# Performance work log

Hardware: AMD Instinct MI355X
Metric: run time of the kernel (lower is better)

The kernel has to match this reference:

```python
import jax, jax.numpy as jnp
import numpy as np
import math

B, C, H, W = 32, 3, 512, 512
K = 16
OUT_H, OUT_W = 512, 512

def _ctrl_pts(k):
    gs = int(math.sqrt(k))
    lin = jnp.linspace(-1.0, 1.0, gs)
    gy, gx = jnp.meshgrid(lin, lin, indexing='ij')
    return jnp.stack([gx, gy], axis=-1).reshape(-1, 2)

def setup_inputs() -> dict:
    key = jax.random.key(0)
    k1, k2, k3, k4 = jax.random.split(key, 4)
    x = jax.random.normal(k1, (B, C, H, W), jnp.float32)
    conv_w = jax.random.normal(k2, (8, C, 7, 7), jnp.float32) * 0.05
    conv_b = jax.random.normal(k3, (8,), jnp.float32) * 0.05
    fc_w = jax.random.normal(k4, (2 * K, 8), jnp.float32) * 0.01
    fc_b = jnp.asarray(_ctrl_pts(K).reshape(-1))  # module inits bias to ctrl grid
    return {"x": x, "conv_w": conv_w, "conv_b": conv_b, "fc_w": fc_w, "fc_b": fc_b}

def _U(sq):
    # U(r) = r^2 * log(r^2 + 1e-6), expressed with squared distance sq = r^2
    return sq * jnp.log(sq + 1e-6)

def _tps_grid(src, tgt, out_h, out_w):
    # src: [K,2] shared across batch (fixed ctrl grid), tgt: [B,K,2]
    Bb, Kk, _ = tgt.shape
    lin_y = jnp.linspace(-1.0, 1.0, out_h)
    lin_x = jnp.linspace(-1.0, 1.0, out_w)
    gy, gx = jnp.meshgrid(lin_y, lin_x, indexing='ij')
    grid = jnp.stack([gx, gy], axis=-1).reshape(-1, 2)  # [N,2]
    N = out_h * out_w
    # RBF kernel between output grid and source ctrl pts: [N,K]
    d2 = jnp.sum((grid[:, None, :] - src[None, :, :]) ** 2, axis=-1)
    U = _U(d2)
    # TPS system matrix L [K+3,K+3]; src is batch-shared so build it once
    src_d2 = jnp.sum((src[:, None, :] - src[None, :, :]) ** 2, axis=-1)
    P = jnp.concatenate([jnp.ones((Kk, 1)), src], axis=1)  # [K,3]
    L = jnp.zeros((Kk + 3, Kk + 3))
    L = L.at[:Kk, :Kk].set(_U(src_d2))
    L = L.at[:Kk, Kk:].set(P)
    L = L.at[Kk:, :Kk].set(P.T)
    Y = jnp.concatenate([tgt, jnp.zeros((Bb, 3, 2))], axis=1)  # [B,K+3,2]
    Wmat = jnp.linalg.solve(L[None], Y)  # [B,K+3,2]
    Pg = jnp.concatenate([jnp.ones((N, 1)), grid], axis=1)  # [N,3]
    mapped = (jnp.einsum('nk,bkc->bnc', U, Wmat[:, :Kk])
              + jnp.einsum('np,bpc->bnc', Pg, Wmat[:, Kk:]))
    return mapped.reshape(Bb, out_h, out_w, 2)

def _grid_sample(x, grid):
    # bilinear, zero padding, align_corners=False (torch defaults)
    Bb, Cc, Hh, Ww = x.shape
    ix = ((grid[..., 0] + 1.0) * Ww - 1.0) * 0.5
    iy = ((grid[..., 1] + 1.0) * Hh - 1.0) * 0.5
    x0 = jnp.floor(ix)
    y0 = jnp.floor(iy)
    wx1 = ix - x0
    wy1 = iy - y0
    x0i = x0.astype(jnp.int32)
    y0i = y0.astype(jnp.int32)

    def gather(img, yy, xx):
        valid = ((yy >= 0) & (yy < Hh) & (xx >= 0) & (xx < Ww)).astype(img.dtype)
        yc = jnp.clip(yy, 0, Hh - 1)
        xc = jnp.clip(xx, 0, Ww - 1)
        return img[:, yc, xc] * valid[None]

    def per(img, x0i, y0i, wx1, wy1):
        wx0 = 1.0 - wx1
        wy0 = 1.0 - wy1
        v00 = gather(img, y0i, x0i)
        v01 = gather(img, y0i, x0i + 1)
        v10 = gather(img, y0i + 1, x0i)
        v11 = gather(img, y0i + 1, x0i + 1)
        return (v00 * (wy0 * wx0)[None] + v01 * (wy0 * wx1)[None]
                + v10 * (wy1 * wx0)[None] + v11 * (wy1 * wx1)[None])

    return jax.vmap(per)(x, x0i, y0i, wx1, wy1)

def reference(x, conv_w, conv_b, fc_w, fc_b):
    # localization: conv7x7 -> relu -> global avg pool -> fc
    feat = jax.lax.conv_general_dilated(
        x, conv_w, window_strides=(1, 1), padding='VALID',
        dimension_numbers=('NCHW', 'OIHW', 'NCHW'))
    feat = jax.nn.relu(feat + conv_b[None, :, None, None])
    pooled = feat.mean(axis=(2, 3))  # [B,8] (AdaptiveAvgPool2d(1))
    pred = (pooled @ fc_w.T + fc_b).reshape(-1, K, 2)  # [B,K,2]
    src = _ctrl_pts(K)
    grid = _tps_grid(src, pred, OUT_H, OUT_W)  # [B,OUT_H,OUT_W,2]
    return _grid_sample(x, grid)
```

## Files before the change

kernel.cpp:

```cpp
#include <hip/hip_runtime.h>
#include <hip/hip_bf16.h>
#include <hip/hip_fp16.h>
#include <math.h>

#define BATCH 32
#define CH_IN 3
#define CH_OUT 8
#define IMG 512
#define KSZ 7
#define CONV_OUT 506
#define KPTS 16
#define TILES_PER_B 128

#define SROWS 23
#define ROW_U4 24
#define ROW_BYTES 384
#define DATA_U4 19
#define SMEM_DW (CH_IN * SROWS * ROW_U4 * 4)
#define NCHUNK (CH_IN * SROWS * ROW_U4)

#define BPB 8

typedef _Float16 half8_t __attribute__((ext_vector_type(8)));
typedef float f32x4_t __attribute__((ext_vector_type(4)));

__device__ __forceinline__ unsigned short f2h_bits(float f) {
    _Float16 h = (_Float16)f;
    unsigned short u;
    __builtin_memcpy(&u, &h, 2);
    return u;
}
__device__ __forceinline__ float h2f_bits(unsigned short u) {
    _Float16 h;
    __builtin_memcpy(&h, &u, 2);
    return (float)h;
}
__device__ __forceinline__ unsigned int pk2(float a, float b) {
    return (unsigned int)f2h_bits(a) | ((unsigned int)f2h_bits(b) << 16);
}

__global__ void wprep_kernel(const float* __restrict__ w, uint4* __restrict__ afrag) {
    int idx = blockIdx.x * 256 + threadIdx.x;
    if (idx >= 6 * 64) return;
    int s = idx >> 6, l = idx & 63;
    int m = l & 15;
    int dlt = m >> 3, o = m & 7;
    int oct = s * 4 + (l >> 4);
    int c = oct >> 3, ky = oct & 7;
    unsigned short h[8];
    #pragma unroll
    for (int j = 0; j < 8; ++j) {
        int kx = j - dlt;
        float v = 0.f;
        if (ky < KSZ && kx >= 0 && kx < KSZ)
            v = w[((o * CH_IN + c) * KSZ + ky) * KSZ + kx];
        h[j] = f2h_bits(v);
    }
    uint4 out;
    __builtin_memcpy(&out, h, 16);
    afrag[idx] = out;
}

template <bool FUSED>
__global__ __launch_bounds__(256)
void conv_pool_kernel(const float* __restrict__ x, unsigned short* __restrict__ xh,
                      const uint4* __restrict__ afrag, const float* __restrict__ conv_b,
                      float* __restrict__ partial) {
    __shared__ unsigned int smem[SMEM_DW];
    __shared__ float red[4][8];

    int blk = blockIdx.x;
    int b = blk >> 7;
    int stripe = (blk >> 2) & 31;
    int chunk = blk & 3;
    int ybase = stripe * 16;
    int x0 = chunk * 128;
    int tid = threadIdx.x;

    {
        const float* xb = x + (size_t)b * CH_IN * IMG * IMG;
        unsigned short* xhb = xh + (size_t)b * CH_IN * IMG * IMG;
        for (int idx4 = tid; idx4 < NCHUNK; idx4 += 256) {
            int c = idx4 / (SROWS * ROW_U4);
            int rem = idx4 - c * (SROWS * ROW_U4);
            int r = rem / ROW_U4;
            int u4 = rem - r * ROW_U4;
            int grow = ybase + r;
            int gcol = x0 + (u4 << 3);
            uint4 v = make_uint4(0u, 0u, 0u, 0u);
            if (u4 < DATA_U4 && grow < IMG && gcol < IMG) {
                const float* rp = xb + ((size_t)c * IMG + grow) * IMG + gcol;
                float4 f0 = *(const float4*)rp;
                float4 f1 = *(const float4*)(rp + 4);
                v.x = pk2(f0.x, f0.y);
                v.y = pk2(f0.z, f0.w);
                v.z = pk2(f1.x, f1.y);
                v.w = pk2(f1.z, f1.w);
            }
            int row = c * SROWS + r;
            *(uint4*)((char*)smem + row * ROW_BYTES + ((u4 ^ (row & 7)) << 4)) = v;
            if (FUSED && r < 16 && u4 < 16)
                *(uint4*)(xhb + ((size_t)c * IMG + grow) * IMG + gcol) = v;
        }
    }
    __syncthreads();

    int l = tid & 63, w = tid >> 6;
    int n = l & 15, g = l >> 4;

    uint4 at[6];
    #pragma unroll
    for (int s = 0; s < 6; ++s) at[s] = afrag[s * 64 + l];

    int rowB[6], rxb[6];
    #pragma unroll
    for (int s = 0; s < 6; ++s) {
        int oct = s * 4 + g;
        int c = oct >> 3, ky = oct & 7;
        int row = c * SROWS + n + ky;
        rowB[s] = row * ROW_BYTES;
        rxb[s] = (row & 7) << 4;
    }

    float bias_[4];
    {
        int ob = (g & 1) * 4;
        #pragma unroll
        for (int r2 = 0; r2 < 4; ++r2) bias_[r2] = conv_b[ob + r2];
    }
    bool rowok = (ybase + n) < CONV_OUT;
    int dlt = g >> 1;
    float sums[4] = {0.f, 0.f, 0.f, 0.f};
    const char* sb = (const char*)smem;

    #pragma unroll
    for (int u = 0; u < 4; ++u) {
        f32x4_t acc[4];
        #pragma unroll
        for (int d = 0; d < 4; ++d) acc[d] = (f32x4_t){0.f, 0.f, 0.f, 0.f};

        int k0 = (4 * w + u) << 4;
        #pragma unroll
        for (int s = 0; s < 6; ++s) {
            uint4 lo = *(const uint4*)(sb + rowB[s] + (k0 ^ rxb[s]));
            uint4 hi = *(const uint4*)(sb + rowB[s] + ((k0 + 16) ^ rxb[s]));
            unsigned int eu[8] = {lo.x, lo.y, lo.z, lo.w, hi.x, hi.y, hi.z, hi.w};
            half8_t a;
            __builtin_memcpy(&a, &at[s], 16);
            #pragma unroll
            for (int d = 0; d < 4; ++d) {
                uint4 bu = make_uint4(eu[d], eu[d + 1], eu[d + 2], eu[d + 3]);
                half8_t bf;
                __builtin_memcpy(&bf, &bu, 16);
                acc[d] = __builtin_amdgcn_mfma_f32_16x16x32_f16(a, bf, acc[d], 0, 0, 0);
            }
        }

        #pragma unroll
        for (int d = 0; d < 4; ++d) {
            int col = x0 + 32 * w + 8 * u + 2 * d + dlt;
            bool colok = col < CONV_OUT;
            #pragma unroll
            for (int r2 = 0; r2 < 4; ++r2) {
                float v = acc[d][r2] + bias_[r2];
                v = v > 0.f ? v : 0.f;
                sums[r2] += (rowok && colok) ? v : 0.f;
            }
        }
    }

    #pragma unroll
    for (int r2 = 0; r2 < 4; ++r2) {
        sums[r2] += __shfl_xor(sums[r2], 1, 64);
        sums[r2] += __shfl_xor(sums[r2], 2, 64);
        sums[r2] += __shfl_xor(sums[r2], 4, 64);
        sums[r2] += __shfl_xor(sums[r2], 8, 64);
        sums[r2] += __shfl_xor(sums[r2], 32, 64);
    }
    if (l == 0) {
        #pragma unroll
        for (int r2 = 0; r2 < 4; ++r2) red[w][r2] = sums[r2];
    }
    if (l == 16) {
        #pragma unroll
        for (int r2 = 0; r2 < 4; ++r2) red[w][4 + r2] = sums[r2];
    }
    __syncthreads();
    if (tid < CH_OUT) {
        float s = red[0][tid] + red[1][tid] + red[2][tid] + red[3][tid];
        partial[tid * (BATCH * TILES_PER_B) + b * TILES_PER_B + stripe * 4 + chunk] = s;
    }
}

__device__ __forceinline__ double ctrl_lin(int i) { return -1.0 + (2.0 / 3.0) * i; }

__global__ void solve_kernel(const float* __restrict__ partial,
                             const float* __restrict__ fc_w,
                             const float* __restrict__ fc_b,
                             float* __restrict__ Wf) {
    __shared__ double L[19][19];
    __shared__ double Ys[19][64];
    __shared__ double piv_fac[19];
    __shared__ int piv_idx;
    __shared__ float pooledS[BATCH][CH_OUT];

    int t = threadIdx.x;

    for (int p = t; p < BATCH * CH_OUT; p += 64) {
        int b = p >> 3, o = p & 7;
        const float4* pp = (const float4*)(partial + o * (BATCH * TILES_PER_B) + b * TILES_PER_B);
        double a0 = 0.0, a1 = 0.0, a2 = 0.0, a3 = 0.0;
        #pragma unroll
        for (int gq = 0; gq < TILES_PER_B / 4; ++gq) {
            float4 v = pp[gq];
            a0 += (double)v.x; a1 += (double)v.y;
            a2 += (double)v.z; a3 += (double)v.w;
        }
        pooledS[b][o] = (float)(((a0 + a1) + (a2 + a3)) / ((double)CONV_OUT * (double)CONV_OUT));
    }
    __syncthreads();

    {
        int b = t >> 1, c = t & 1;
        for (int k = 0; k < KPTS; ++k) {
            int j = k * 2 + c;
            double s = (double)fc_b[j];
            for (int o = 0; o < CH_OUT; ++o)
                s += (double)pooledS[b][o] * (double)fc_w[j * CH_OUT + o];
            Ys[k][t] = s;
        }
        for (int k = KPTS; k < 19; ++k) Ys[k][t] = 0.0;
    }

    for (int p = t; p < 19 * 19; p += 64) {
        int r = p / 19, cc = p % 19;
        double v;
        if (r < KPTS && cc < KPTS) {
            double dx = ctrl_lin(r & 3) - ctrl_lin(cc & 3);
            double dy = ctrl_lin(r >> 2) - ctrl_lin(cc >> 2);
            double d2 = dx * dx + dy * dy;
            v = d2 * log(d2 + 1e-6);
        } else if (r < KPTS) {
            v = (cc == KPTS) ? 1.0 : (cc == KPTS + 1 ? ctrl_lin(r & 3) : ctrl_lin(r >> 2));
        } else if (cc < KPTS) {
            v = (r == KPTS) ? 1.0 : (r == KPTS + 1 ? ctrl_lin(cc & 3) : ctrl_lin(cc >> 2));
        } else v = 0.0;
        L[r][cc] = v;
    }
    __syncthreads();

    for (int k = 0; k < 19; ++k) {
        if (t == 0) {
            int pi = k; double mx = fabs(L[k][k]);
            for (int i = k + 1; i < 19; ++i) {
                double a = fabs(L[i][k]);
                if (a > mx) { mx = a; pi = i; }
            }
            piv_idx = pi;
        }
        __syncthreads();
        int pi = piv_idx;
        if (pi != k) {
            if (t < 19) { double tmp = L[k][t]; L[k][t] = L[pi][t]; L[pi][t] = tmp; }
            { double tmp = Ys[k][t]; Ys[k][t] = Ys[pi][t]; Ys[pi][t] = tmp; }
        }
        __syncthreads();
        if (t > k && t < 19) piv_fac[t] = L[t][k] / L[k][k];
        __syncthreads();
        if (t > k && t < 19) {
            double lkj = L[k][t];
            for (int i = k + 1; i < 19; ++i) L[i][t] -= piv_fac[i] * lkj;
        }
        {
            double ykt = Ys[k][t];
            for (int i = k + 1; i < 19; ++i) Ys[i][t] -= piv_fac[i] * ykt;
        }
        __syncthreads();
    }

    for (int k = 18; k >= 0; --k) {
        double s = Ys[k][t];
        for (int j = k + 1; j < 19; ++j) s -= L[k][j] * Ys[j][t];
        Ys[k][t] = s / L[k][k];
    }

    {
        int b = t >> 1, c = t & 1;
        for (int k = 0; k < 19; ++k)
            Wf[(b * 19 + k) * 2 + c] = (float)Ys[k][t];
    }
}

template <bool H16>
__global__ __launch_bounds__(256)
void tps_sample_kernel(const float* __restrict__ x, const unsigned short* __restrict__ xh,
                       const float* __restrict__ Wf, float* __restrict__ out) {
    int blk = blockIdx.x;
    int bgrp = blk >> 10;
    int pix = ((blk & 1023) << 8) | threadIdx.x;
    int i = pix >> 9, j = pix & 511;

    float gx = -1.f + (2.f / 511.f) * (float)j;
    float gy = -1.f + (2.f / 511.f) * (float)i;

    float U[KPTS];
    #pragma unroll
    for (int k = 0; k < KPTS; ++k) {
        float sx = -1.f + (2.f / 3.f) * (float)(k & 3);
        float sy = -1.f + (2.f / 3.f) * (float)(k >> 2);
        float dx = gx - sx, dy = gy - sy;
        float d2 = dx * dx + dy * dy;
        U[k] = d2 * (0.69314718055994531f * __log2f(d2 + 1e-6f));
    }

    for (int b = bgrp * BPB; b < bgrp * BPB + BPB; ++b) {
        const float* Wb = Wf + b * 38;

        float mx = Wb[32] + gx * Wb[34] + gy * Wb[36];
        float my = Wb[33] + gx * Wb[35] + gy * Wb[37];
        #pragma unroll
        for (int k = 0; k < KPTS; ++k) {
            mx += U[k] * Wb[2 * k];
            my += U[k] * Wb[2 * k + 1];
        }

        float ix = (mx + 1.f) * 256.f - 0.5f;
        float iy = (my + 1.f) * 256.f - 0.5f;
        float x0f = floorf(ix), y0f = floorf(iy);
        int x0 = (int)x0f, y0 = (int)y0f;
        int x1 = x0 + 1, y1 = y0 + 1;
        float wx1 = ix - x0f, wy1 = iy - y0f;
        float wx0 = 1.f - wx1, wy0 = 1.f - wy1;

        bool vx0 = (x0 >= 0) & (x0 < IMG), vx1 = (x1 >= 0) & (x1 < IMG);
        bool vy0 = (y0 >= 0) & (y0 < IMG), vy1 = (y1 >= 0) & (y1 < IMG);
        int xc0 = min(max(x0, 0), IMG - 1), xc1 = min(max(x1, 0), IMG - 1);
        int yc0 = min(max(y0, 0), IMG - 1), yc1 = min(max(y1, 0), IMG - 1);

        float w00 = (vy0 && vx0) ? wy0 * wx0 : 0.f;
        float w01 = (vy0 && vx1) ? wy0 * wx1 : 0.f;
        float w10 = (vy1 && vx0) ? wy1 * wx0 : 0.f;
        float w11 = (vy1 && vx1) ? wy1 * wx1 : 0.f;

        int o00 = yc0 * IMG + xc0, o01 = yc0 * IMG + xc1;
        int o10 = yc1 * IMG + xc0, o11 = yc1 * IMG + xc1;

        #pragma unroll
        for (int c = 0; c < CH_IN; ++c) {
            float v;
            if (H16) {
                const unsigned short* xp = xh + ((size_t)b * CH_IN + c) * IMG * IMG;
                v = h2f_bits(xp[o00]) * w00 + h2f_bits(xp[o01]) * w01
                  + h2f_bits(xp[o10]) * w10 + h2f_bits(xp[o11]) * w11;
            } else {
                const float* xp = x + ((size_t)b * CH_IN + c) * IMG * IMG;
                v = xp[o00] * w00 + xp[o01] * w01 + xp[o10] * w10 + xp[o11] * w11;
            }
            out[(((size_t)b * CH_IN + c) << 18) + (i << 9) + j] = v;
        }
    }
}

extern "C" void kernel_launch(void* const* d_in, const int* in_sizes, int n_in,
                              void* d_out, int out_size, void* d_ws, size_t ws_size,
                              hipStream_t stream) {
    const float* x      = (const float*)d_in[0];
    const float* conv_w = (const float*)d_in[1];
    const float* conv_b = (const float*)d_in[2];
    const float* fc_w   = (const float*)d_in[3];
    const float* fc_b   = (const float*)d_in[4];
    float* out = (float*)d_out;

    char* ws = (char*)d_ws;
    uint4* afrag   = (uint4*)ws;
    float* partial = (float*)(ws + 8192);
    float* Wf      = (float*)(ws + 139264);
    unsigned short* xh = (unsigned short*)(ws + 147456);
    const size_t need = 147456 + (size_t)BATCH * CH_IN * IMG * IMG * 2;
    bool fused = ws_size >= need;

    wprep_kernel<<<dim3(2), dim3(256), 0, stream>>>(conv_w, afrag);
    if (fused) {
        conv_pool_kernel<true><<<dim3(BATCH * TILES_PER_B), dim3(256), 0, stream>>>(
            x, xh, afrag, conv_b, partial);
    } else {
        conv_pool_kernel<false><<<dim3(BATCH * TILES_PER_B), dim3(256), 0, stream>>>(
            x, xh, afrag, conv_b, partial);
    }
    solve_kernel<<<dim3(1), dim3(64), 0, stream>>>(partial, fc_w, fc_b, Wf);
    if (fused) {
        tps_sample_kernel<true><<<dim3(4 * 1024), dim3(256), 0, stream>>>(x, xh, Wf, out);
    } else {
        tps_sample_kernel<false><<<dim3(4 * 1024), dim3(256), 0, stream>>>(x, xh, Wf, out);
    }
}
```

Measured before the change: 157.3 us.

## Widen conv tiles to 256 columns and replace XOR swizzle with padded rows

Each conv/pool block now covers a 16x256 stripe instead of 16x128, which halves the block count and cuts the halo columns reloaded per tile. The XOR-swizzled LDS layout is replaced by rows padded to 528 bytes, which avoids bank conflicts with simpler addressing, and each wave runs two column chunks per block. The partial-sum indexing and the per-batch tile count are updated to match. The cost is more LDS per block and fewer blocks, so there is less parallelism to hide load latency.

```diff
diff --git a/kernel.cpp b/kernel.cpp
--- a/kernel.cpp
+++ b/kernel.cpp
@@ -10,13 +10,13 @@
 #define KSZ 7
 #define CONV_OUT 506
 #define KPTS 16
-#define TILES_PER_B 128
+#define TILES_PER_B 64
 
 #define SROWS 23
-#define ROW_U4 24
-#define ROW_BYTES 384
-#define DATA_U4 19
-#define SMEM_DW (CH_IN * SROWS * ROW_U4 * 4)
+#define ROW_PX 264
+#define ROW_U4 33
+#define ROW_BYTES 528
+#define SMEM_DW (CH_IN * SROWS * (ROW_BYTES / 4))
 #define NCHUNK (CH_IN * SROWS * ROW_U4)
 
 #define BPB 8
@@ -70,11 +70,12 @@
     __shared__ float red[4][8];
 
     int blk = blockIdx.x;
-    int b = blk >> 7;
-    int stripe = (blk >> 2) & 31;
-    int chunk = blk & 3;
+    int b = blk >> 6;
+    int rem0 = blk & 63;
+    int stripe = rem0 >> 1;
+    int half = rem0 & 1;
     int ybase = stripe * 16;
-    int x0 = chunk * 128;
+    int x0 = half * 256;
     int tid = threadIdx.x;
 
     {
@@ -88,7 +89,7 @@
             int grow = ybase + r;
             int gcol = x0 + (u4 << 3);
             uint4 v = make_uint4(0u, 0u, 0u, 0u);
-            if (u4 < DATA_U4 && grow < IMG && gcol < IMG) {
+            if (grow < IMG && gcol < IMG) {
                 const float* rp = xb + ((size_t)c * IMG + grow) * IMG + gcol;
                 float4 f0 = *(const float4*)rp;
                 float4 f1 = *(const float4*)(rp + 4);
@@ -97,9 +98,8 @@
                 v.z = pk2(f1.x, f1.y);
                 v.w = pk2(f1.z, f1.w);
             }
-            int row = c * SROWS + r;
-            *(uint4*)((char*)smem + row * ROW_BYTES + ((u4 ^ (row & 7)) << 4)) = v;
-            if (FUSED && r < 16 && u4 < 16)
+            *(uint4*)((char*)smem + (c * SROWS + r) * ROW_BYTES + (u4 << 4)) = v;
+            if (FUSED && r < 16 && u4 < 32)
                 *(uint4*)(xhb + ((size_t)c * IMG + grow) * IMG + gcol) = v;
         }
     }
@@ -112,14 +112,12 @@
     #pragma unroll
     for (int s = 0; s < 6; ++s) at[s] = afrag[s * 64 + l];
 
-    int rowB[6], rxb[6];
+    int rowb[6];
     #pragma unroll
     for (int s = 0; s < 6; ++s) {
         int oct = s * 4 + g;
         int c = oct >> 3, ky = oct & 7;
-        int row = c * SROWS + n + ky;
-        rowB[s] = row * ROW_BYTES;
-        rxb[s] = (row & 7) << 4;
+        rowb[s] = (c * SROWS + n + ky) * ROW_BYTES + w * 64;
     }
 
     float bias_[4];
@@ -134,37 +132,40 @@
     const char* sb = (const char*)smem;
 
     #pragma unroll
-    for (int u = 0; u < 4; ++u) {
-        f32x4_t acc[4];
-        #pragma unroll
-        for (int d = 0; d < 4; ++d) acc[d] = (f32x4_t){0.f, 0.f, 0.f, 0.f};
-
-        int k0 = (4 * w + u) << 4;
-        #pragma unroll
-        for (int s = 0; s < 6; ++s) {
-            uint4 lo = *(const uint4*)(sb + rowB[s] + (k0 ^ rxb[s]));
-            uint4 hi = *(const uint4*)(sb + rowB[s] + ((k0 + 16) ^ rxb[s]));
-            unsigned int eu[8] = {lo.x, lo.y, lo.z, lo.w, hi.x, hi.y, hi.z, hi.w};
-            half8_t a;
-            __builtin_memcpy(&a, &at[s], 16);
+    for (int cc = 0; cc < 2; ++cc) {
+        int off = cc * 256;
+        #pragma unroll
+        for (int u = 0; u < 4; ++u) {
+            f32x4_t acc[4];
+            #pragma unroll
+            for (int d = 0; d < 4; ++d) acc[d] = (f32x4_t){0.f, 0.f, 0.f, 0.f};
+
+            #pragma unroll
+            for (int s = 0; s < 6; ++s) {
+                uint4 lo = *(const uint4*)(sb + rowb[s] + off + (u << 4));
+                uint4 hi = *(const uint4*)(sb + rowb[s] + off + (u << 4) + 16);
+                unsigned int eu[8] = {lo.x, lo.y, lo.z, lo.w, hi.x, hi.y, hi.z, hi.w};
+                half8_t a;
+                __builtin_memcpy(&a, &at[s], 16);
+                #pragma unroll
+                for (int d = 0; d < 4; ++d) {
+                    uint4 bu = make_uint4(eu[d], eu[d + 1], eu[d + 2], eu[d + 3]);
+                    half8_t bf;
+                    __builtin_memcpy(&bf, &bu, 16);
+                    acc[d] = __builtin_amdgcn_mfma_f32_16x16x32_f16(a, bf, acc[d], 0, 0, 0);
+                }
+            }
+
             #pragma unroll
             for (int d = 0; d < 4; ++d) {
-                uint4 bu = make_uint4(eu[d], eu[d + 1], eu[d + 2], eu[d + 3]);
-                half8_t bf;
-                __builtin_memcpy(&bf, &bu, 16);
-                acc[d] = __builtin_amdgcn_mfma_f32_16x16x32_f16(a, bf, acc[d], 0, 0, 0);
-            }
-        }
-
-        #pragma unroll
-        for (int d = 0; d < 4; ++d) {
-            int col = x0 + 32 * w + 8 * u + 2 * d + dlt;
-            bool colok = col < CONV_OUT;
-            #pragma unroll
-            for (int r2 = 0; r2 < 4; ++r2) {
-                float v = acc[d][r2] + bias_[r2];
-                v = v > 0.f ? v : 0.f;
-                sums[r2] += (rowok && colok) ? v : 0.f;
+                int col = x0 + cc * 128 + 32 * w + 8 * u + 2 * d + dlt;
+                bool colok = col < CONV_OUT;
+                #pragma unroll
+                for (int r2 = 0; r2 < 4; ++r2) {
+                    float v = acc[d][r2] + bias_[r2];
+                    v = v > 0.f ? v : 0.f;
+                    sums[r2] += (rowok && colok) ? v : 0.f;
+                }
             }
         }
     }
@@ -188,7 +189,7 @@
     __syncthreads();
     if (tid < CH_OUT) {
         float s = red[0][tid] + red[1][tid] + red[2][tid] + red[3][tid];
-        partial[tid * (BATCH * TILES_PER_B) + b * TILES_PER_B + stripe * 4 + chunk] = s;
+        partial[tid * (BATCH * TILES_PER_B) + b * TILES_PER_B + stripe * 2 + half] = s;
     }
 }
 
```

Result: faster. 141.4 us (median of 2 runs) (-10.1%).
